# Kernel optimization log

Measured on AMD Instinct MI355X. Metric: run time of the kernel, lower is better.

## Reference

```python
import jax, jax.numpy as jnp
import numpy as np


def _make_cameras(key, B):
    """Well-conditioned c = [cam2world(16), intrinsics(9)] per batch."""
    k1, k2 = jax.random.split(key)
    # random rotation via Gram-Schmidt on a random 3x3
    A = jax.random.normal(k1, (B, 3, 3), dtype=jnp.float32)
    q0 = A[:, :, 0] / jnp.linalg.norm(A[:, :, 0], axis=-1, keepdims=True)
    v1 = A[:, :, 1] - jnp.sum(A[:, :, 1] * q0, -1, keepdims=True) * q0
    q1 = v1 / jnp.linalg.norm(v1, axis=-1, keepdims=True)
    q2 = jnp.cross(q0, q1)
    R = jnp.stack([q0, q1, q2], axis=-1)                      # [B,3,3]
    t = 2.7 * q2                                              # camera at radius 2.7 along view axis
    cam2world = jnp.zeros((B, 4, 4), jnp.float32)
    cam2world = cam2world.at[:, :3, :3].set(R)
    cam2world = cam2world.at[:, :3, 3].set(t)
    cam2world = cam2world.at[:, 3, 3].set(1.0)
    # EG3D-style normalized intrinsics: fx=fy=4.2647, cx=cy=0.5, sk=0
    intr = jnp.tile(jnp.array([[4.2647, 0.0, 0.5],
                               [0.0, 4.2647, 0.5],
                               [0.0, 0.0, 1.0]], jnp.float32), (B, 1, 1))
    return jnp.concatenate([cam2world.reshape(B, 16), intr.reshape(B, 9)], axis=1)


def setup_inputs() -> dict:
    key = jax.random.key(0)
    kc, kd, kp = jax.random.split(key, 3)
    B, R, M = 8, 64, 4096
    c = _make_cameras(kc, B)
    image_depth = 2.2 + 1.1 * jax.random.uniform(kd, (B, R * R, 1), dtype=jnp.float32)
    pc = 0.3 * jax.random.normal(kp, (B, M, 3), dtype=jnp.float32)
    return {"c": c, "image_depth": image_depth, "pc": pc, "resolution": R}


def _ray_sampler(cam2world, intrinsics, resolution):
    B = cam2world.shape[0]
    N = resolution * resolution
    fx = intrinsics[:, 0, 0][:, None]
    fy = intrinsics[:, 1, 1][:, None]
    cx = intrinsics[:, 0, 2][:, None]
    cy = intrinsics[:, 1, 2][:, None]
    sk = intrinsics[:, 0, 1][:, None]
    r = (jnp.arange(resolution, dtype=jnp.float32) + 0.5) / resolution
    gi, gj = jnp.meshgrid(r, r, indexing='ij')                # row, col
    x_cam = jnp.broadcast_to(gj.reshape(-1), (B, N))          # uv.flip(0): x is col coord
    y_cam = jnp.broadcast_to(gi.reshape(-1), (B, N))
    z_cam = jnp.ones((B, N), jnp.float32)
    x_lift = (x_cam - cx + cy * sk / fy - sk * y_cam / fy) / fx * z_cam
    y_lift = (y_cam - cy) / fy * z_cam
    cam_rel = jnp.stack([x_lift, y_lift, z_cam, jnp.ones_like(z_cam)], axis=-1)  # [B,N,4]
    world = jnp.einsum('bij,bnj->bni', cam2world, cam_rel)[..., :3]
    origins = cam2world[:, :3, 3]                              # [B,3]
    dirs = world - origins[:, None, :]
    dirs = dirs / jnp.linalg.norm(dirs, axis=-1, keepdims=True)
    ray_origins = jnp.broadcast_to(origins[:, None, :], dirs.shape)
    return ray_origins, dirs


def _chamfer(x, y):
    # squared-distance NN both directions; GEMM-form pairwise distances
    x2 = jnp.sum(x * x, axis=-1)                               # [B,N]
    y2 = jnp.sum(y * y, axis=-1)                               # [B,M]
    xy = jnp.einsum('bnd,bmd->bnm', x, y)                      # [B,N,M]
    d = x2[:, :, None] + y2[:, None, :] - 2.0 * xy
    return jnp.min(d, axis=2), jnp.min(d, axis=1)              # dist1 [B,N], dist2 [B,M]


def reference(c, image_depth, pc, resolution):
    B = c.shape[0]
    pc = pc[..., :3]
    depth = image_depth.reshape(B, -1, 1)
    cam2world = c[:, :16].reshape(-1, 4, 4)
    intr = c[:, 16:25].reshape(-1, 3, 3)
    ro, rd = _ray_sampler(cam2world, intr, resolution)
    pred_pos = depth * rd + ro                                  # [B,N,3]
    d0, d1 = _chamfer(pred_pos, pc)
    K = min(pred_pos.shape[1], pc.shape[1]) // 2
    d0s = jnp.sort(d0, axis=1)[:, :K]
    d1s = d0s  # NOTE: faithful to original code (loss_1_sorted is assigned from loss_0_sorted)
    loss0 = jnp.mean(d0s, axis=1)
    loss1 = jnp.mean(d1s, axis=1)
    return (loss0 + loss1).reshape(B, 1)
```

## Files before the change

kernel.cpp:

```cpp
#include <hip/hip_runtime.h>
#include <math.h>

#define FLT_BIG 3.0e38f
#define HIST_BINS 16384

typedef short short8 __attribute__((ext_vector_type(8)));
typedef float floatx4 __attribute__((ext_vector_type(4)));
typedef float floatx16 __attribute__((ext_vector_type(16)));

union U4S8 { uint4 u; short8 s; };

static __device__ __forceinline__ unsigned int f2bf(float f) {
    unsigned int u = __float_as_uint(f);
    return (u + 0x7FFFu + ((u >> 16) & 1u)) >> 16;
}
static __device__ __forceinline__ float bf2f(unsigned int b) {
    return __uint_as_float(b << 16);
}

__global__ __launch_bounds__(256, 2) void chamfer_mfma_kernel(
    const float* __restrict__ cparam,
    const float* __restrict__ depth,
    const float* __restrict__ pc,
    float* __restrict__ d0,
    int N, int M, int R)
{
    const int b    = blockIdx.y;
    const int tid  = threadIdx.x;
    const int lane = tid & 63;
    const int wv   = tid >> 6;
    const int row  = lane & 31;
    const int half = lane >> 5;

    extern __shared__ uint4 sld[];
    __shared__ float smin[4][32];

    const float* pcb = pc + (size_t)b * M * 3;
    const int Ms = M >> 8;
    for (int s = 0; s < Ms; s++) {
        const int idx = s * 256 + tid;
        const float x = pcb[idx * 3 + 0];
        const float y = pcb[idx * 3 + 1];
        const float z = pcb[idx * 3 + 2];
        const float hq = 0.5f * (x * x + y * y + z * z);
        uint4 u;
        u.x = f2bf(x) | (f2bf(y) << 16);
        u.y = f2bf(z) | (f2bf(hq) << 16);
        u.z = 0x3F803F80u;
        u.w = 0u;
        sld[idx] = u;
    }
    __syncthreads();

    const float* cb = cparam + (size_t)b * 25;
    const float fx = cb[16], sk = cb[17], cx = cb[18];
    const float fy = cb[20], cy = cb[21];

    const int nbase = blockIdx.x * 64;
    const int n  = nbase + (wv & 1) * 32 + row;
    const int i0 = n / R;
    const int j0 = n - i0 * R;
    const float x_cam = (j0 + 0.5f) / (float)R;
    const float y_cam = (i0 + 0.5f) / (float)R;
    const float x_lift = (x_cam - cx + cy * sk / fy - sk * y_cam / fy) / fx;
    const float y_lift = (y_cam - cy) / fy;
    const float dxw = cb[0] * x_lift + cb[1] * y_lift + cb[2];
    const float dyw = cb[4] * x_lift + cb[5] * y_lift + cb[6];
    const float dzw = cb[8] * x_lift + cb[9] * y_lift + cb[10];
    const float inv = 1.0f / sqrtf(dxw * dxw + dyw * dyw + dzw * dzw);
    const float dep = depth[(size_t)b * N + n];
    const float px = cb[3]  + dep * dxw * inv;
    const float py = cb[7]  + dep * dyw * inv;
    const float pz = cb[11] + dep * dzw * inv;

    const float hp = 0.5f * (px * px + py * py + pz * pz);
    const unsigned int hp_hi = f2bf(hp);
    const unsigned int hp_lo = f2bf(hp - bf2f(hp_hi));

    U4S8 af;
    af.u = make_uint4(0u, 0u, 0u, 0u);
    if (half == 0) {
        af.u.x = f2bf(-px) | (f2bf(-py) << 16);
        af.u.y = f2bf(-pz) | (0x3F80u << 16);
        af.u.z = hp_hi | (hp_lo << 16);
    }
    const short8 afrag = af.s;
    const floatx16 zero16 = {0,0,0,0,0,0,0,0,0,0,0,0,0,0,0,0};

    float minsA[16], minsB[16];
    #pragma unroll
    for (int t = 0; t < 16; t++) { minsA[t] = FLT_BIG; minsB[t] = FLT_BIG; }

    const int fbase = (wv >> 1) * 64;
    for (int f = 0; f < 64; f += 8) {
        uint4 bu[8];
        #pragma unroll
        for (int mm = 0; mm < 8; mm++)
            bu[mm] = sld[((fbase + f + mm) << 5) + row];
        #pragma unroll
        for (int mm = 0; mm < 8; mm++) {
            U4S8 bf; bf.u = bu[mm];
            floatx16 d = __builtin_amdgcn_mfma_f32_32x32x16_bf16(
                             afrag, bf.s, zero16, 0, 0, 0);
            if (mm & 1) {
                #pragma unroll
                for (int t = 0; t < 16; t++) minsB[t] = fminf(minsB[t], d[t]);
            } else {
                #pragma unroll
                for (int t = 0; t < 16; t++) minsA[t] = fminf(minsA[t], d[t]);
            }
        }
    }

    #pragma unroll
    for (int t = 0; t < 16; t++) {
        float v = fminf(minsA[t], minsB[t]);
        v = fminf(v, __shfl_xor(v, 1));
        v = fminf(v, __shfl_xor(v, 2));
        v = fminf(v, __shfl_xor(v, 4));
        v = fminf(v, __shfl_xor(v, 8));
        v = fminf(v, __shfl_xor(v, 16));
        minsA[t] = v;
    }
    if (row == 0) {
        #pragma unroll
        for (int t = 0; t < 16; t++)
            smin[wv][(t & 3) + 8 * (t >> 2) + 4 * half] = minsA[t];
    }
    __syncthreads();

    if (tid < 64) {
        const int g  = tid >> 5;
        const int rr = tid & 31;
        const float v = fminf(smin[g][rr], smin[g + 2][rr]);
        d0[(size_t)b * N + nbase + tid] = fmaxf(2.0f * v, 0.0f);
    }
}

__global__ __launch_bounds__(256, 1) void select_mean_kernel(
    const float* __restrict__ d0,
    float* __restrict__ out,
    int N, int K)
{
    const int b   = blockIdx.x;
    const int tid = threadIdx.x;

    extern __shared__ unsigned int hist[];
    __shared__ unsigned int spart[256];
    __shared__ unsigned int s_selbin, s_krem;
    __shared__ unsigned int subcnt[32];
    __shared__ float        subsum[32];
    __shared__ float        s_below;

    for (int t2 = tid; t2 < HIST_BINS; t2 += 256) hist[t2] = 0u;
    if (tid < 32) { subcnt[tid] = 0u; subsum[tid] = 0.0f; }
    if (tid == 0) s_below = 0.0f;
    __syncthreads();

    unsigned int key[16];
    #pragma unroll
    for (int t2 = 0; t2 < 16; t2++)
        key[t2] = __float_as_uint(d0[(size_t)b * N + t2 * 256 + tid]);
    #pragma unroll
    for (int t2 = 0; t2 < 16; t2++)
        atomicAdd(&hist[key[t2] >> 18], 1u);
    __syncthreads();

    unsigned int psum = 0u;
    #pragma unroll 8
    for (int i2 = 0; i2 < 64; i2++)
        psum += hist[(tid << 6) + ((i2 + tid) & 63)];
    spart[tid] = psum;
    __syncthreads();

    unsigned int cbef = 0u;
    for (int i2 = 0; i2 < tid; i2++) cbef += spart[i2];
    if (cbef < (unsigned int)K && (unsigned int)K <= cbef + psum) {
        unsigned int k2 = (unsigned int)K - cbef;
        unsigned int sel = 0u;
        for (int i2 = 0; i2 < 64; i2++) {
            unsigned int h = hist[(tid << 6) + i2];
            if (k2 <= h) { sel = (tid << 6) + i2; break; }
            k2 -= h;
        }
        s_selbin = sel;
        s_krem   = k2;
    }
    __syncthreads();

    const unsigned int selbin = s_selbin;
    float sumb = 0.0f;
    #pragma unroll
    for (int t2 = 0; t2 < 16; t2++) {
        const unsigned int bin = key[t2] >> 18;
        const float v = __uint_as_float(key[t2]);
        if (bin < selbin) sumb += v;
        if (bin == selbin) {
            const unsigned int sub = (key[t2] >> 13) & 31u;
            atomicAdd(&subcnt[sub], 1u);
            atomicAdd(&subsum[sub], v);
        }
    }
    atomicAdd(&s_below, sumb);
    __syncthreads();

    if (tid == 0) {
        unsigned int k2 = s_krem;
        float s = s_below;
        for (int i2 = 0; i2 < 32; i2++) {
            unsigned int h = subcnt[i2];
            if (k2 <= h) {
                s += (h ? (subsum[i2] * ((float)k2 / (float)h)) : 0.0f);
                break;
            }
            s += subsum[i2];
            k2 -= h;
        }
        out[b] = 2.0f * s / (float)K;
    }
}

extern "C" void kernel_launch(void* const* d_in, const int* in_sizes, int n_in,
                              void* d_out, int out_size, void* d_ws, size_t ws_size,
                              hipStream_t stream)
{
    const float* c   = (const float*)d_in[0];
    const float* dep = (const float*)d_in[1];
    const float* pc  = (const float*)d_in[2];
    float* out = (float*)d_out;

    const int B = in_sizes[0] / 25;
    const int N = in_sizes[1] / B;
    const int M = in_sizes[2] / (3 * B);
    int R = 1; while (R * R < N) R++;

    float* d0 = (float*)d_ws;

    dim3 gridA(N / 64, B);
    size_t ldsA = (size_t)M * sizeof(uint4);
    hipLaunchKernelGGL(chamfer_mfma_kernel, gridA, dim3(256), ldsA, stream,
                       c, dep, pc, d0, N, M, R);

    const int K = ((N < M) ? N : M) / 2;
    size_t ldsB = (size_t)HIST_BINS * sizeof(unsigned int);
    hipLaunchKernelGGL(select_mean_kernel, dim3(B), dim3(256), ldsB, stream,
                       d0, out, N, K);
}
```

Baseline: 82.23 us.

## Fuse top-K selection into chamfer kernel via last-block-done counter

Merges the separate select/mean kernel into the chamfer kernel. Each block bumps a per-batch atomic counter after writing its d0 values, and the last block to finish a batch reuses the LDS buffer as the histogram and runs the selection and mean. This removes one dependent kernel launch and its tail gap, but adds a small zeroing kernel, thread fences, and a serialized selection tail on the last block of each batch.

```diff
diff --git a/kernel.cpp b/kernel.cpp
--- a/kernel.cpp
+++ b/kernel.cpp
@@ -5,7 +5,6 @@
 #define HIST_BINS 16384
 
 typedef short short8 __attribute__((ext_vector_type(8)));
-typedef float floatx4 __attribute__((ext_vector_type(4)));
 typedef float floatx16 __attribute__((ext_vector_type(16)));
 
 union U4S8 { uint4 u; short8 s; };
@@ -18,12 +17,19 @@
     return __uint_as_float(b << 16);
 }
 
-__global__ __launch_bounds__(256, 2) void chamfer_mfma_kernel(
+__global__ void zero_cnt_kernel(unsigned int* __restrict__ cnt, int B)
+{
+    if ((int)threadIdx.x < B) cnt[threadIdx.x] = 0u;
+}
+
+__global__ __launch_bounds__(256, 2) void chamfer_fused_kernel(
     const float* __restrict__ cparam,
     const float* __restrict__ depth,
     const float* __restrict__ pc,
     float* __restrict__ d0,
-    int N, int M, int R)
+    unsigned int* __restrict__ cnt,
+    float* __restrict__ out,
+    int N, int M, int R, int K)
 {
     const int b    = blockIdx.y;
     const int tid  = threadIdx.x;
@@ -34,6 +40,12 @@
 
     extern __shared__ uint4 sld[];
     __shared__ float smin[4][32];
+    __shared__ int   s_last;
+    __shared__ unsigned int spart[256];
+    __shared__ unsigned int s_selbin, s_krem;
+    __shared__ unsigned int subcnt[32];
+    __shared__ float        subsum[32];
+    __shared__ float        s_below;
 
     const float* pcb = pc + (size_t)b * M * 3;
     const int Ms = M >> 8;
@@ -135,22 +147,18 @@
         const float v = fminf(smin[g][rr], smin[g + 2][rr]);
         d0[(size_t)b * N + nbase + tid] = fmaxf(2.0f * v, 0.0f);
     }
-}
-
-__global__ __launch_bounds__(256, 1) void select_mean_kernel(
-    const float* __restrict__ d0,
-    float* __restrict__ out,
-    int N, int K)
-{
-    const int b   = blockIdx.x;
-    const int tid = threadIdx.x;
-
-    extern __shared__ unsigned int hist[];
-    __shared__ unsigned int spart[256];
-    __shared__ unsigned int s_selbin, s_krem;
-    __shared__ unsigned int subcnt[32];
-    __shared__ float        subsum[32];
-    __shared__ float        s_below;
+
+    __threadfence();
+    __syncthreads();
+    if (tid == 0) {
+        const unsigned int done = atomicAdd(&cnt[b], 1u);
+        s_last = (done == gridDim.x - 1) ? 1 : 0;
+    }
+    __syncthreads();
+    if (!s_last) return;
+
+    __threadfence();
+    unsigned int* hist = (unsigned int*)sld;
 
     for (int t2 = tid; t2 < HIST_BINS; t2 += 256) hist[t2] = 0u;
     if (tid < 32) { subcnt[tid] = 0u; subsum[tid] = 0.0f; }
@@ -233,16 +241,18 @@
     const int N = in_sizes[1] / B;
     const int M = in_sizes[2] / (3 * B);
     int R = 1; while (R * R < N) R++;
+    const int K = ((N < M) ? N : M) / 2;
 
     float* d0 = (float*)d_ws;
-
-    dim3 gridA(N / 64, B);
+    unsigned int* cnt = (unsigned int*)((char*)d_ws + (size_t)B * N * sizeof(float));
+
+    hipLaunchKernelGGL(zero_cnt_kernel, dim3(1), dim3(64), 0, stream, cnt, B);
+
     size_t ldsA = (size_t)M * sizeof(uint4);
-    hipLaunchKernelGGL(chamfer_mfma_kernel, gridA, dim3(256), ldsA, stream,
-                       c, dep, pc, d0, N, M, R);
-
-    const int K = ((N < M) ? N : M) / 2;
-    size_t ldsB = (size_t)HIST_BINS * sizeof(unsigned int);
-    hipLaunchKernelGGL(select_mean_kernel, dim3(B), dim3(256), ldsB, stream,
-                       d0, out, N, K);
-}
+    size_t ldsH = (size_t)HIST_BINS * sizeof(unsigned int);
+    size_t lds  = ldsA > ldsH ? ldsA : ldsH;
+
+    dim3 grid(N / 64, B);
+    hipLaunchKernelGGL(chamfer_fused_kernel, grid, dim3(256), lds, stream,
+                       c, dep, pc, d0, cnt, out, N, M, R, K);
+}
```

Measured after the change: 111.4 us. +35.5%, slower.

## Pre-pack point-cloud fragments in a separate kernel and stream them from global memory

Applied to the files above, without the earlier changes.

Adds a small kernel that converts the point cloud to packed bf16 MFMA B-fragments once per batch and writes them to the workspace. The chamfer kernel no longer rebuilds these fragments into LDS in every block. It reads them straight from global/L2 memory, covers 32 rays per block, and has each wave scan a quarter of the points. This removes the redundant per-block packing and LDS staging and raises occupancy. The cost is one extra kernel launch and more global/L2 traffic, since every block now rereads the fragments.

```diff
diff --git a/kernel.cpp b/kernel.cpp
--- a/kernel.cpp
+++ b/kernel.cpp
@@ -5,7 +5,6 @@
 #define HIST_BINS 16384
 
 typedef short short8 __attribute__((ext_vector_type(8)));
-typedef float floatx4 __attribute__((ext_vector_type(4)));
 typedef float floatx16 __attribute__((ext_vector_type(16)));
 
 union U4S8 { uint4 u; short8 s; };
@@ -18,10 +17,29 @@
     return __uint_as_float(b << 16);
 }
 
-__global__ __launch_bounds__(256, 2) void chamfer_mfma_kernel(
+__global__ __launch_bounds__(256) void pack_frags_kernel(
+    const float* __restrict__ pc,
+    uint4* __restrict__ frags,
+    int total)
+{
+    const int idx = blockIdx.x * 256 + threadIdx.x;
+    if (idx >= total) return;
+    const float x = pc[idx * 3 + 0];
+    const float y = pc[idx * 3 + 1];
+    const float z = pc[idx * 3 + 2];
+    const float hq = 0.5f * (x * x + y * y + z * z);
+    uint4 u;
+    u.x = f2bf(x) | (f2bf(y) << 16);
+    u.y = f2bf(z) | (f2bf(hq) << 16);
+    u.z = 0x3F803F80u;
+    u.w = 0u;
+    frags[idx] = u;
+}
+
+__global__ __launch_bounds__(256, 4) void chamfer_mfma_kernel(
     const float* __restrict__ cparam,
     const float* __restrict__ depth,
-    const float* __restrict__ pc,
+    const uint4* __restrict__ frags,
     float* __restrict__ d0,
     int N, int M, int R)
 {
@@ -32,32 +50,14 @@
     const int row  = lane & 31;
     const int half = lane >> 5;
 
-    extern __shared__ uint4 sld[];
     __shared__ float smin[4][32];
-
-    const float* pcb = pc + (size_t)b * M * 3;
-    const int Ms = M >> 8;
-    for (int s = 0; s < Ms; s++) {
-        const int idx = s * 256 + tid;
-        const float x = pcb[idx * 3 + 0];
-        const float y = pcb[idx * 3 + 1];
-        const float z = pcb[idx * 3 + 2];
-        const float hq = 0.5f * (x * x + y * y + z * z);
-        uint4 u;
-        u.x = f2bf(x) | (f2bf(y) << 16);
-        u.y = f2bf(z) | (f2bf(hq) << 16);
-        u.z = 0x3F803F80u;
-        u.w = 0u;
-        sld[idx] = u;
-    }
-    __syncthreads();
 
     const float* cb = cparam + (size_t)b * 25;
     const float fx = cb[16], sk = cb[17], cx = cb[18];
     const float fy = cb[20], cy = cb[21];
 
-    const int nbase = blockIdx.x * 64;
-    const int n  = nbase + (wv & 1) * 32 + row;
+    const int nbase = blockIdx.x * 32;
+    const int n  = nbase + row;
     const int i0 = n / R;
     const int j0 = n - i0 * R;
     const float x_cam = (j0 + 0.5f) / (float)R;
@@ -91,12 +91,12 @@
     #pragma unroll
     for (int t = 0; t < 16; t++) { minsA[t] = FLT_BIG; minsB[t] = FLT_BIG; }
 
-    const int fbase = (wv >> 1) * 64;
-    for (int f = 0; f < 64; f += 8) {
+    const uint4* fb = frags + (size_t)b * M + (wv << 10);
+    for (int f = 0; f < 32; f += 8) {
         uint4 bu[8];
         #pragma unroll
         for (int mm = 0; mm < 8; mm++)
-            bu[mm] = sld[((fbase + f + mm) << 5) + row];
+            bu[mm] = fb[((f + mm) << 5) + row];
         #pragma unroll
         for (int mm = 0; mm < 8; mm++) {
             U4S8 bf; bf.u = bu[mm];
@@ -129,10 +129,9 @@
     }
     __syncthreads();
 
-    if (tid < 64) {
-        const int g  = tid >> 5;
-        const int rr = tid & 31;
-        const float v = fminf(smin[g][rr], smin[g + 2][rr]);
+    if (tid < 32) {
+        const float v = fminf(fminf(smin[0][tid], smin[1][tid]),
+                              fminf(smin[2][tid], smin[3][tid]));
         d0[(size_t)b * N + nbase + tid] = fmaxf(2.0f * v, 0.0f);
     }
 }
@@ -233,15 +232,19 @@
     const int N = in_sizes[1] / B;
     const int M = in_sizes[2] / (3 * B);
     int R = 1; while (R * R < N) R++;
-
-    float* d0 = (float*)d_ws;
-
-    dim3 gridA(N / 64, B);
-    size_t ldsA = (size_t)M * sizeof(uint4);
-    hipLaunchKernelGGL(chamfer_mfma_kernel, gridA, dim3(256), ldsA, stream,
-                       c, dep, pc, d0, N, M, R);
-
     const int K = ((N < M) ? N : M) / 2;
+
+    float* d0    = (float*)d_ws;
+    uint4* frags = (uint4*)((char*)d_ws + (size_t)B * N * sizeof(float));
+
+    const int total = B * M;
+    hipLaunchKernelGGL(pack_frags_kernel, dim3((total + 255) / 256), dim3(256),
+                       0, stream, pc, frags, total);
+
+    dim3 gridA(N / 32, B);
+    hipLaunchKernelGGL(chamfer_mfma_kernel, gridA, dim3(256), 0, stream,
+                       c, dep, frags, d0, N, M, R);
+
     size_t ldsB = (size_t)HIST_BINS * sizeof(unsigned int);
     hipLaunchKernelGGL(select_mean_kernel, dim3(B), dim3(256), ldsB, stream,
                        d0, out, N, K);
```

Result: no change. 82.62 us (+0.5%).

## Use 1024-thread blocks over 128 rays with compact 8-byte LDS point storage

Applied to the files above, without the earlier changes.

The chamfer kernel now launches 1024-thread blocks that each cover 128 ray points. The work is split into 4 row groups times 4 point quarters, and the per-wave results are min-reduced across 16 slots in shared memory. Point-cloud entries in LDS shrink from 16 to 8 bytes, with the constant ones padding rebuilt in registers. This halves LDS footprint and LDS read traffic and halves the number of times each block stages the point cloud. In exchange the blocks are larger, with a single sync point, and the launch-bounds occupancy hint is dropped.

```diff
diff --git a/kernel.cpp b/kernel.cpp
--- a/kernel.cpp
+++ b/kernel.cpp
@@ -5,7 +5,6 @@
 #define HIST_BINS 16384
 
 typedef short short8 __attribute__((ext_vector_type(8)));
-typedef float floatx4 __attribute__((ext_vector_type(4)));
 typedef float floatx16 __attribute__((ext_vector_type(16)));
 
 union U4S8 { uint4 u; short8 s; };
@@ -18,7 +17,7 @@
     return __uint_as_float(b << 16);
 }
 
-__global__ __launch_bounds__(256, 2) void chamfer_mfma_kernel(
+__global__ __launch_bounds__(1024) void chamfer_mfma_kernel(
     const float* __restrict__ cparam,
     const float* __restrict__ depth,
     const float* __restrict__ pc,
@@ -29,35 +28,34 @@
     const int tid  = threadIdx.x;
     const int lane = tid & 63;
     const int wv   = tid >> 6;
+    const int rg   = wv & 3;
+    const int mq   = wv >> 2;
     const int row  = lane & 31;
     const int half = lane >> 5;
 
-    extern __shared__ uint4 sld[];
-    __shared__ float smin[4][32];
+    extern __shared__ uint2 sld[];
+    __shared__ float smin[16][32];
 
     const float* pcb = pc + (size_t)b * M * 3;
-    const int Ms = M >> 8;
+    const int Ms = M >> 10;
     for (int s = 0; s < Ms; s++) {
-        const int idx = s * 256 + tid;
+        const int idx = (s << 10) + tid;
         const float x = pcb[idx * 3 + 0];
         const float y = pcb[idx * 3 + 1];
         const float z = pcb[idx * 3 + 2];
         const float hq = 0.5f * (x * x + y * y + z * z);
-        uint4 u;
+        uint2 u;
         u.x = f2bf(x) | (f2bf(y) << 16);
         u.y = f2bf(z) | (f2bf(hq) << 16);
-        u.z = 0x3F803F80u;
-        u.w = 0u;
         sld[idx] = u;
     }
-    __syncthreads();
 
     const float* cb = cparam + (size_t)b * 25;
     const float fx = cb[16], sk = cb[17], cx = cb[18];
     const float fy = cb[20], cy = cb[21];
 
-    const int nbase = blockIdx.x * 64;
-    const int n  = nbase + (wv & 1) * 32 + row;
+    const int nbase = blockIdx.x * 128;
+    const int n  = nbase + rg * 32 + row;
     const int i0 = n / R;
     const int j0 = n - i0 * R;
     const float x_cam = (j0 + 0.5f) / (float)R;
@@ -91,15 +89,18 @@
     #pragma unroll
     for (int t = 0; t < 16; t++) { minsA[t] = FLT_BIG; minsB[t] = FLT_BIG; }
 
-    const int fbase = (wv >> 1) * 64;
-    for (int f = 0; f < 64; f += 8) {
-        uint4 bu[8];
+    __syncthreads();
+
+    const int fbo = mq << 10;
+    for (int f = 0; f < 32; f += 8) {
+        uint2 bu[8];
         #pragma unroll
         for (int mm = 0; mm < 8; mm++)
-            bu[mm] = sld[((fbase + f + mm) << 5) + row];
+            bu[mm] = sld[fbo + ((f + mm) << 5) + row];
         #pragma unroll
         for (int mm = 0; mm < 8; mm++) {
-            U4S8 bf; bf.u = bu[mm];
+            U4S8 bf;
+            bf.u = make_uint4(bu[mm].x, bu[mm].y, 0x3F803F80u, 0u);
             floatx16 d = __builtin_amdgcn_mfma_f32_32x32x16_bf16(
                              afrag, bf.s, zero16, 0, 0, 0);
             if (mm & 1) {
@@ -129,10 +130,11 @@
     }
     __syncthreads();
 
-    if (tid < 64) {
-        const int g  = tid >> 5;
-        const int rr = tid & 31;
-        const float v = fminf(smin[g][rr], smin[g + 2][rr]);
+    if (tid < 128) {
+        const int rg2 = tid >> 5;
+        const int rr  = tid & 31;
+        const float v = fminf(fminf(smin[rg2][rr],      smin[rg2 + 4][rr]),
+                              fminf(smin[rg2 + 8][rr],  smin[rg2 + 12][rr]));
         d0[(size_t)b * N + nbase + tid] = fmaxf(2.0f * v, 0.0f);
     }
 }
@@ -233,15 +235,15 @@
     const int N = in_sizes[1] / B;
     const int M = in_sizes[2] / (3 * B);
     int R = 1; while (R * R < N) R++;
+    const int K = ((N < M) ? N : M) / 2;
 
     float* d0 = (float*)d_ws;
 
-    dim3 gridA(N / 64, B);
-    size_t ldsA = (size_t)M * sizeof(uint4);
-    hipLaunchKernelGGL(chamfer_mfma_kernel, gridA, dim3(256), ldsA, stream,
+    dim3 gridA(N / 128, B);
+    size_t ldsA = (size_t)M * sizeof(uint2);
+    hipLaunchKernelGGL(chamfer_mfma_kernel, gridA, dim3(1024), ldsA, stream,
                        c, dep, pc, d0, N, M, R);
 
-    const int K = ((N < M) ? N : M) / 2;
     size_t ldsB = (size_t)HIST_BINS * sizeof(unsigned int);
     hipLaunchKernelGGL(select_mean_kernel, dim3(B), dim3(256), ldsB, stream,
                        d0, out, N, K);
```

Measured after the change: 81.66 us. Within noise of the previous version (-0.7%).
